# Performance work log

Measured on AMD Instinct MI355X. Metric: run time of the kernel, lower is better.

The kernel has to match this reference:

```python
import jax, jax.numpy as jnp
import numpy as np

B, S, D, H = 2, 2048, 1024, 16
HD = D // H  # head_dim = 64


def setup_inputs() -> dict:
    key = jax.random.key(0)
    ks = jax.random.split(key, 10)
    scale = 0.02
    return {
        "features": jax.random.normal(ks[0], (B, S, D), dtype=jnp.float32),
        "attention_mask": jnp.zeros((B, 1, S, S), dtype=jnp.float32),
        "wq": jax.random.normal(ks[1], (D, D), dtype=jnp.float32) * scale,
        "bq": jnp.zeros((D,), dtype=jnp.float32),
        "wk": jax.random.normal(ks[2], (D, D), dtype=jnp.float32) * scale,
        "bk": jnp.zeros((D,), dtype=jnp.float32),
        "wv": jax.random.normal(ks[3], (D, D), dtype=jnp.float32) * scale,
        "bv": jnp.zeros((D,), dtype=jnp.float32),
        "wo": jax.random.normal(ks[4], (D, D), dtype=jnp.float32) * scale,
        "bo": jnp.zeros((D,), dtype=jnp.float32),
    }


def _split_heads(x):
    # [B,S,D] -> [B,H,S,HD]
    return x.reshape(B, S, H, HD).transpose(0, 2, 1, 3)


def reference(features, attention_mask, wq, bq, wk, bk, wv, bv, wo, bo):
    scaling = HD ** -0.5
    # torch Linear: y = x @ W.T + b; Bart scales q by head_dim**-0.5
    q = _split_heads((features @ wq.T + bq) * scaling)
    k = _split_heads(features @ wk.T + bk)
    v = _split_heads(features @ wv.T + bv)
    scores = jnp.einsum("bhqd,bhkd->bhqk", q, k) + attention_mask
    attn = jax.nn.softmax(scores, axis=-1)
    ctx = jnp.einsum("bhqk,bhkd->bhqd", attn, v)
    ctx = ctx.transpose(0, 2, 1, 3).reshape(B, S, D)
    gated = ctx @ wo.T + bo
    out = features * gated
    return (out, gated)
```

## Files before the change

### kernel.cpp

```cpp
#include <hip/hip_runtime.h>
#include <math.h>

#define Bc 2
#define Sc 2048
#define Dc 1024
#define Hc 16
#define HDc 64
#define NROWS 4096

typedef __attribute__((ext_vector_type(8))) _Float16 f16x8;
typedef __attribute__((ext_vector_type(4))) _Float16 f16x4;
typedef __attribute__((ext_vector_type(2))) __fp16 fp16v2;
typedef __attribute__((ext_vector_type(4))) float f32x4;
typedef __attribute__((ext_vector_type(16))) float f32x16;

__global__ __launch_bounds__(256)
void cvt5(const float* __restrict__ f,  const float* __restrict__ wq,
          const float* __restrict__ wk, const float* __restrict__ wv,
          const float* __restrict__ wo_,
          _Float16* __restrict__ fh, _Float16* __restrict__ wh3,
          _Float16* __restrict__ woh)
{
  int blk = blockIdx.x;
  const float* src; _Float16* hi; int base;
  if (blk < 4096)      { src = f;   hi = fh;            base = blk; }
  else if (blk < 5120) { src = wq;  hi = wh3;           base = blk - 4096; }
  else if (blk < 6144) { src = wk;  hi = wh3 + 1048576; base = blk - 5120; }
  else if (blk < 7168) { src = wv;  hi = wh3 + 2097152; base = blk - 6144; }
  else                 { src = wo_; hi = woh;           base = blk - 7168; }
  int i = base * 256 + threadIdx.x;
  float4 v = reinterpret_cast<const float4*>(src)[i];
  f16x4 h;
  h[0] = (_Float16)v.x; h[1] = (_Float16)v.y;
  h[2] = (_Float16)v.z; h[3] = (_Float16)v.w;
  reinterpret_cast<f16x4*>(hi)[i] = h;
}

__global__ __launch_bounds__(256)
void mask_scan(const float* __restrict__ m, unsigned int* __restrict__ flag)
{
  int i = blockIdx.x * 256 + threadIdx.x;
  float4 v = reinterpret_cast<const float4*>(m)[i];
  bool nz = (v.x != 0.f) || (v.y != 0.f) || (v.z != 0.f) || (v.w != 0.f);
  if (__any(nz)) {
    if ((threadIdx.x & 63) == 0) atomicOr(flag, 1u);
  }
}

__global__ __launch_bounds__(256, 4)
void gemm_qkv(const _Float16* __restrict__ Ah, const _Float16* __restrict__ Wh,
              const float* __restrict__ bq, const float* __restrict__ bk,
              const float* __restrict__ bv,
              _Float16* __restrict__ qb, _Float16* __restrict__ kb,
              _Float16* __restrict__ vtb)
{
  __shared__ _Float16 Ash[128][40];
  __shared__ _Float16 Wsh[128][40];

  const int tid  = threadIdx.x;
  const int lane = tid & 63, wid = tid >> 6;
  const int l15  = lane & 15, l4 = lane >> 4;
  const int wr   = wid >> 1, wc = wid & 1;
  const int arow0 = blockIdx.x * 128;
  const int wrow0 = blockIdx.y * 128;

  f32x4 acc[4][4];
#pragma unroll
  for (int m = 0; m < 4; ++m)
#pragma unroll
    for (int n = 0; n < 4; ++n) acc[m][n] = f32x4{0.f, 0.f, 0.f, 0.f};

  for (int k0 = 0; k0 < Dc; k0 += 32) {
    __syncthreads();
#pragma unroll
    for (int p = 0; p < 2; ++p) {
      int e = tid + 256 * p;
      int r = e >> 2, c8 = (e & 3) * 8;
      *reinterpret_cast<uint4*>(&Ash[r][c8]) =
          *reinterpret_cast<const uint4*>(Ah + (size_t)(arow0 + r) * Dc + k0 + c8);
      *reinterpret_cast<uint4*>(&Wsh[r][c8]) =
          *reinterpret_cast<const uint4*>(Wh + (size_t)(wrow0 + r) * Dc + k0 + c8);
    }
    __syncthreads();

    f16x8 bh[4];
#pragma unroll
    for (int n = 0; n < 4; ++n)
      bh[n] = *reinterpret_cast<const f16x8*>(&Wsh[wc * 64 + n * 16 + l15][l4 * 8]);
#pragma unroll
    for (int m = 0; m < 4; ++m) {
      f16x8 ah = *reinterpret_cast<const f16x8*>(&Ash[wr * 64 + m * 16 + l15][l4 * 8]);
#pragma unroll
      for (int n = 0; n < 4; ++n)
        acc[m][n] = __builtin_amdgcn_mfma_f32_16x16x32_f16(ah, bh[n], acc[m][n], 0, 0, 0);
    }
  }

#pragma unroll
  for (int m = 0; m < 4; ++m) {
#pragma unroll
    for (int n = 0; n < 4; ++n) {
      int cbase = wrow0 + wc * 64 + n * 16;
      int seg = cbase >> 10;
      int o = (cbase & 1023) + l15;
      int h = o >> 6, hd = o & 63;
      const float* bias = (seg == 0) ? bq : ((seg == 1) ? bk : bv);
      float bval = bias[o];
      float alpha = (seg == 0) ? 0.125f : 1.0f;
      int r0 = arow0 + wr * 64 + m * 16 + l4 * 4;
      int b = r0 >> 11, s0 = r0 & (Sc - 1);
      if (seg == 2) {
        f16x4 pk;
#pragma unroll
        for (int reg = 0; reg < 4; ++reg)
          pk[reg] = (_Float16)((acc[m][n][reg] + bval) * alpha);
        *reinterpret_cast<f16x4*>(
            &vtb[(((size_t)b * Hc + h) * HDc + hd) * Sc + s0]) = pk;
      } else {
        _Float16* dst = (seg == 0) ? qb : kb;
#pragma unroll
        for (int reg = 0; reg < 4; ++reg) {
          float val = (acc[m][n][reg] + bval) * alpha;
          dst[(((size_t)b * Hc + h) * Sc + (s0 + reg)) * HDc + hd] = (_Float16)val;
        }
      }
    }
  }
}

__global__ __launch_bounds__(256, 4)
void gemm_wo(const _Float16* __restrict__ Ah, const _Float16* __restrict__ Wh,
             const float* __restrict__ bias,
             float* __restrict__ out0, float* __restrict__ out1,
             const float* __restrict__ feats)
{
  __shared__ _Float16 Ash[64][40];
  __shared__ _Float16 Wsh[128][40];

  const int tid  = threadIdx.x;
  const int lane = tid & 63, wid = tid >> 6;
  const int l15  = lane & 15, l4 = lane >> 4;
  const int wr   = wid >> 1, wc = wid & 1;
  const int arow0 = blockIdx.x * 64;
  const int wrow0 = blockIdx.y * 128;

  f32x4 acc[2][4];
#pragma unroll
  for (int m = 0; m < 2; ++m)
#pragma unroll
    for (int n = 0; n < 4; ++n) acc[m][n] = f32x4{0.f, 0.f, 0.f, 0.f};

  for (int k0 = 0; k0 < Dc; k0 += 32) {
    __syncthreads();
    {
      int r = tid >> 2, c8 = (tid & 3) * 8;
      *reinterpret_cast<uint4*>(&Ash[r][c8]) =
          *reinterpret_cast<const uint4*>(Ah + (size_t)(arow0 + r) * Dc + k0 + c8);
    }
#pragma unroll
    for (int p = 0; p < 2; ++p) {
      int e = tid + 256 * p;
      int r = e >> 2, c8 = (e & 3) * 8;
      *reinterpret_cast<uint4*>(&Wsh[r][c8]) =
          *reinterpret_cast<const uint4*>(Wh + (size_t)(wrow0 + r) * Dc + k0 + c8);
    }
    __syncthreads();

    f16x8 bh[4];
#pragma unroll
    for (int n = 0; n < 4; ++n)
      bh[n] = *reinterpret_cast<const f16x8*>(&Wsh[wc * 64 + n * 16 + l15][l4 * 8]);
#pragma unroll
    for (int m = 0; m < 2; ++m) {
      f16x8 ah = *reinterpret_cast<const f16x8*>(&Ash[wr * 32 + m * 16 + l15][l4 * 8]);
#pragma unroll
      for (int n = 0; n < 4; ++n)
        acc[m][n] = __builtin_amdgcn_mfma_f32_16x16x32_f16(ah, bh[n], acc[m][n], 0, 0, 0);
    }
  }

#pragma unroll
  for (int m = 0; m < 2; ++m) {
#pragma unroll
    for (int n = 0; n < 4; ++n) {
      int c = wrow0 + wc * 64 + n * 16 + l15;
      float bval = bias[c];
#pragma unroll
      for (int reg = 0; reg < 4; ++reg) {
        int r = arow0 + wr * 32 + m * 16 + l4 * 4 + reg;
        float val = acc[m][n][reg] + bval;
        out1[(size_t)r * Dc + c] = val;
        out0[(size_t)r * Dc + c] = feats[(size_t)r * Dc + c] * val;
      }
    }
  }
}

#define QB 128
#define KB 64
#define NT (Sc / KB)

__global__ __launch_bounds__(256, 2)
void attn_mfma(const _Float16* __restrict__ q,
               const _Float16* __restrict__ k,
               const _Float16* __restrict__ vt,
               const float* __restrict__ mask,
               const unsigned int* __restrict__ mflag,
               _Float16* __restrict__ ctxh)
{
  __shared__ _Float16 Ks[2][KB * 64];
  __shared__ _Float16 Vs[2][HDc * 64];

  const int tid  = threadIdx.x;
  const int lane = tid & 63;
  const int wq   = tid >> 6;
  const int l31  = lane & 31;
  const int hi   = lane >> 5;

  const int nqb  = Sc / QB;
  const int bid  = blockIdx.x;
  const int swz  = (bid & 7) * 64 + (bid >> 3);
  const int head = swz / nqb;
  const int q0   = (swz % nqb) * QB;
  const int b    = head / Hc;
  const int h    = head % Hc;

  const bool use_mask = (*mflag != 0u);

  const _Float16* kbase  = k  + (size_t)head * Sc * HDc;
  const _Float16* vtbase = vt + (size_t)head * HDc * Sc;
  const _Float16* qbase  = q  + ((size_t)head * Sc + q0 + wq * 32 + l31) * HDc;
  const float*    ml     = mask + ((size_t)b * Sc + q0 + wq * 32 + l31) * Sc + 4 * hi;

  const int r0s = tid >> 3, cs = tid & 7;
  const int r1s = r0s + 32;
  const int so0 = r0s * 64 + ((cs ^ (r0s & 7)) * 8);
  const int so1 = r1s * 64 + ((cs ^ (r1s & 7)) * 8);

  f16x8 qf[4];
#pragma unroll
  for (int c = 0; c < 4; ++c)
    qf[c] = *reinterpret_cast<const f16x8*>(qbase + hi * 8 + 16 * c);

  f16x8 ones;
#pragma unroll
  for (int i = 0; i < 8; ++i) ones[i] = (_Float16)1.0f;

  f32x16 O0, O1, lacc;
#pragma unroll
  for (int i = 0; i < 16; ++i) { O0[i] = 0.f; O1[i] = 0.f; lacc[i] = 0.f; }
  float m_q = -3e38f;

  *reinterpret_cast<uint4*>(&Ks[0][so0]) =
      *reinterpret_cast<const uint4*>(kbase + (size_t)r0s * HDc + cs * 8);
  *reinterpret_cast<uint4*>(&Ks[0][so1]) =
      *reinterpret_cast<const uint4*>(kbase + (size_t)r1s * HDc + cs * 8);
  *reinterpret_cast<uint4*>(&Vs[0][so0]) =
      *reinterpret_cast<const uint4*>(vtbase + (size_t)r0s * Sc + cs * 8);
  *reinterpret_cast<uint4*>(&Vs[0][so1]) =
      *reinterpret_cast<const uint4*>(vtbase + (size_t)r1s * Sc + cs * 8);
  float4 mpf[8];
  if (use_mask) {
#pragma unroll
    for (int t2 = 0; t2 < 2; ++t2)
#pragma unroll
      for (int j = 0; j < 4; ++j)
        mpf[t2 * 4 + j] = *reinterpret_cast<const float4*>(ml + 32 * t2 + 8 * j);
  }

  for (int kt = 0; kt < NT; ++kt) {
    const int k0 = kt * KB;
    const int cur = kt & 1, nxt = cur ^ 1;
    __syncthreads();

    uint4 kr0, kr1, vr0, vr1;
    const bool pf = (kt + 1) < NT;
    if (pf) {
      const int k1 = k0 + KB;
      kr0 = *reinterpret_cast<const uint4*>(kbase + (size_t)(k1 + r0s) * HDc + cs * 8);
      kr1 = *reinterpret_cast<const uint4*>(kbase + (size_t)(k1 + r1s) * HDc + cs * 8);
      vr0 = *reinterpret_cast<const uint4*>(vtbase + (size_t)r0s * Sc + k1 + cs * 8);
      vr1 = *reinterpret_cast<const uint4*>(vtbase + (size_t)r1s * Sc + k1 + cs * 8);
    }

    f32x16 s[2];
    __builtin_amdgcn_s_setprio(1);
#pragma unroll
    for (int t2 = 0; t2 < 2; ++t2) {
      f32x16 acc;
#pragma unroll
      for (int i = 0; i < 16; ++i) acc[i] = 0.f;
      const int krow = t2 * 32 + l31;
#pragma unroll
      for (int c = 0; c < 4; ++c) {
        const int ofs = krow * 64 + (((2 * c + hi) ^ (krow & 7)) * 8);
        acc = __builtin_amdgcn_mfma_f32_32x32x16_f16(
            *reinterpret_cast<const f16x8*>(&Ks[cur][ofs]), qf[c], acc, 0, 0, 0);
      }
      s[t2] = acc;
    }
    __builtin_amdgcn_s_setprio(0);

    if (use_mask) {
#pragma unroll
      for (int t2 = 0; t2 < 2; ++t2)
#pragma unroll
        for (int j = 0; j < 4; ++j) {
          float4 mv = mpf[t2 * 4 + j];
          s[t2][4 * j + 0] += mv.x; s[t2][4 * j + 1] += mv.y;
          s[t2][4 * j + 2] += mv.z; s[t2][4 * j + 3] += mv.w;
        }
      if (pf) {
#pragma unroll
        for (int t2 = 0; t2 < 2; ++t2)
#pragma unroll
          for (int j = 0; j < 4; ++j)
            mpf[t2 * 4 + j] = *reinterpret_cast<const float4*>(
                ml + (k0 + KB) + 32 * t2 + 8 * j);
      }
    }

    float lm = s[0][0];
#pragma unroll
    for (int t2 = 0; t2 < 2; ++t2)
#pragma unroll
      for (int i = 0; i < 16; ++i) lm = fmaxf(lm, s[t2][i]);

    if (!__all(lm - m_q <= 8.0f)) {
      float vm = fmaxf(lm, __shfl_xor(lm, 32));
      float mn = fmaxf(m_q, vm);
      float cc = __expf(m_q - mn);
      m_q = mn;
#pragma unroll
      for (int reg = 0; reg < 16; ++reg) {
        int q_r = (reg & 3) + 8 * (reg >> 2) + 4 * hi;
        float ccr = __shfl(cc, q_r);
        O0[reg] *= ccr; O1[reg] *= ccr; lacc[reg] *= ccr;
      }
    }

    __builtin_amdgcn_s_setprio(1);
#pragma unroll
    for (int c = 0; c < 4; ++c) {
      const int t2 = c >> 1, rb = (c & 1) * 8;
      float p0 = __expf(s[t2][rb + 0] - m_q);
      float p1 = __expf(s[t2][rb + 1] - m_q);
      float p2 = __expf(s[t2][rb + 2] - m_q);
      float p3 = __expf(s[t2][rb + 3] - m_q);
      float p4 = __expf(s[t2][rb + 4] - m_q);
      float p5 = __expf(s[t2][rb + 5] - m_q);
      float p6 = __expf(s[t2][rb + 6] - m_q);
      float p7 = __expf(s[t2][rb + 7] - m_q);
      union { fp16v2 h; unsigned int u; } w0, w1, w2, w3;
      w0.h = __builtin_amdgcn_cvt_pkrtz(p0, p1);
      w1.h = __builtin_amdgcn_cvt_pkrtz(p2, p3);
      w2.h = __builtin_amdgcn_cvt_pkrtz(p4, p5);
      w3.h = __builtin_amdgcn_cvt_pkrtz(p6, p7);
      unsigned int u0 = w0.u, u1 = w1.u, u2 = w2.u, u3 = w3.u;
      asm("v_permlane32_swap_b32 %0, %1" : "+v"(u0), "+v"(u2));
      asm("v_permlane32_swap_b32 %0, %1" : "+v"(u1), "+v"(u3));
      union { unsigned int u[4]; f16x8 f; } pa;
      pa.u[0] = u0; pa.u[1] = u1; pa.u[2] = u2; pa.u[3] = u3;

      lacc = __builtin_amdgcn_mfma_f32_32x32x16_f16(pa.f, ones, lacc, 0, 0, 0);
      const int vofs = l31 * 64 + (((2 * c + hi) ^ (l31 & 7)) * 8);
      O0 = __builtin_amdgcn_mfma_f32_32x32x16_f16(
          pa.f, *reinterpret_cast<const f16x8*>(&Vs[cur][vofs]), O0, 0, 0, 0);
      O1 = __builtin_amdgcn_mfma_f32_32x32x16_f16(
          pa.f, *reinterpret_cast<const f16x8*>(&Vs[cur][vofs + 32 * 64]), O1, 0, 0, 0);
    }
    __builtin_amdgcn_s_setprio(0);

    if (pf) {
      *reinterpret_cast<uint4*>(&Ks[nxt][so0]) = kr0;
      *reinterpret_cast<uint4*>(&Ks[nxt][so1]) = kr1;
      *reinterpret_cast<uint4*>(&Vs[nxt][so0]) = vr0;
      *reinterpret_cast<uint4*>(&Vs[nxt][so1]) = vr1;
    }
  }

#pragma unroll
  for (int reg = 0; reg < 16; ++reg) {
    int q_r = (reg & 3) + 8 * (reg >> 2) + 4 * hi;
    float inv = 1.0f / lacc[reg];
    size_t rowbase = ((size_t)b * Sc + (q0 + wq * 32 + q_r)) * Dc + h * HDc;
    ctxh[rowbase + l31]      = (_Float16)(O0[reg] * inv);
    ctxh[rowbase + 32 + l31] = (_Float16)(O1[reg] * inv);
  }
}

extern "C" void kernel_launch(void* const* d_in, const int* in_sizes, int n_in,
                              void* d_out, int out_size, void* d_ws, size_t ws_size,
                              hipStream_t stream) {
  const float* feats = (const float*)d_in[0];
  const float* mask  = (const float*)d_in[1];
  const float* wq    = (const float*)d_in[2];
  const float* bq    = (const float*)d_in[3];
  const float* wk    = (const float*)d_in[4];
  const float* bk    = (const float*)d_in[5];
  const float* wv    = (const float*)d_in[6];
  const float* bv    = (const float*)d_in[7];
  const float* wo    = (const float*)d_in[8];
  const float* bo    = (const float*)d_in[9];

  char* ws = (char*)d_ws;
  const size_t MB = (size_t)1 << 20;
  _Float16* fh    = (_Float16*)(ws);
  _Float16* wh3   = (_Float16*)(ws + 8  * MB);
  _Float16* woh   = (_Float16*)(ws + 14 * MB);
  _Float16* qb    = (_Float16*)(ws + 16 * MB);
  _Float16* kb    = (_Float16*)(ws + 24 * MB);
  _Float16* vtb   = (_Float16*)(ws + 32 * MB);
  _Float16* ctxh  = (_Float16*)(ws + 40 * MB);
  unsigned int* mflag = (unsigned int*)(ws + 48 * MB);

  float* out   = (float*)d_out;
  float* gated = out + 4194304;

  hipMemsetAsync(mflag, 0, 4, stream);
  mask_scan<<<8192, 256, 0, stream>>>(mask, mflag);

  cvt5<<<8192, 256, 0, stream>>>(feats, wq, wk, wv, wo, fh, wh3, woh);

  gemm_qkv<<<dim3(NROWS / 128, 3072 / 128), 256, 0, stream>>>(
      fh, wh3, bq, bk, bv, qb, kb, vtb);

  attn_mfma<<<Bc * Hc * (Sc / QB), 256, 0, stream>>>(qb, kb, vtb, mask, mflag, ctxh);

  gemm_wo<<<dim3(NROWS / 64, Dc / 128), 256, 0, stream>>>(
      ctxh, woh, bo, out, gated, feats);
}
```

Baseline: 150.1 us.

## Fuse mask scan into conversion kernel and halve attention query block

The mask-nonzero scan is merged into the fp16 conversion kernel, so one launch does both jobs and a kernel boundary goes away. The attention kernel moves from 128-query blocks with 4 waves to 64-query blocks with 2 waves, doubling the grid to 1024 blocks. The block swizzle and the K/V tile load loop change to match, with each thread now loading 4 rows instead of 2. The aim is better CU occupancy and load balance for attention, at the cost of reloading K/V tiles more often per query.

```diff
diff --git a/kernel.cpp b/kernel.cpp
--- a/kernel.cpp
+++ b/kernel.cpp
@@ -15,11 +15,11 @@
 typedef __attribute__((ext_vector_type(16))) float f32x16;
 
 __global__ __launch_bounds__(256)
-void cvt5(const float* __restrict__ f,  const float* __restrict__ wq,
+void prep(const float* __restrict__ f,  const float* __restrict__ wq,
           const float* __restrict__ wk, const float* __restrict__ wv,
-          const float* __restrict__ wo_,
+          const float* __restrict__ wo_, const float* __restrict__ mask,
           _Float16* __restrict__ fh, _Float16* __restrict__ wh3,
-          _Float16* __restrict__ woh)
+          _Float16* __restrict__ woh, unsigned int* __restrict__ flag)
 {
   int blk = blockIdx.x;
   const float* src; _Float16* hi; int base;
@@ -34,14 +34,10 @@
   h[0] = (_Float16)v.x; h[1] = (_Float16)v.y;
   h[2] = (_Float16)v.z; h[3] = (_Float16)v.w;
   reinterpret_cast<f16x4*>(hi)[i] = h;
-}
-
-__global__ __launch_bounds__(256)
-void mask_scan(const float* __restrict__ m, unsigned int* __restrict__ flag)
-{
-  int i = blockIdx.x * 256 + threadIdx.x;
-  float4 v = reinterpret_cast<const float4*>(m)[i];
-  bool nz = (v.x != 0.f) || (v.y != 0.f) || (v.z != 0.f) || (v.w != 0.f);
+
+  int g = blk * 256 + threadIdx.x;
+  float4 mv = reinterpret_cast<const float4*>(mask)[g];
+  bool nz = (mv.x != 0.f) || (mv.y != 0.f) || (mv.z != 0.f) || (mv.w != 0.f);
   if (__any(nz)) {
     if ((threadIdx.x & 63) == 0) atomicOr(flag, 1u);
   }
@@ -196,11 +192,11 @@
   }
 }
 
-#define QB 128
+#define QB 64
 #define KB 64
 #define NT (Sc / KB)
 
-__global__ __launch_bounds__(256, 2)
+__global__ __launch_bounds__(128, 2)
 void attn_mfma(const _Float16* __restrict__ q,
                const _Float16* __restrict__ k,
                const _Float16* __restrict__ vt,
@@ -219,7 +215,7 @@
 
   const int nqb  = Sc / QB;
   const int bid  = blockIdx.x;
-  const int swz  = (bid & 7) * 64 + (bid >> 3);
+  const int swz  = (bid & 7) * 128 + (bid >> 3);
   const int head = swz / nqb;
   const int q0   = (swz % nqb) * QB;
   const int b    = head / Hc;
@@ -232,10 +228,13 @@
   const _Float16* qbase  = q  + ((size_t)head * Sc + q0 + wq * 32 + l31) * HDc;
   const float*    ml     = mask + ((size_t)b * Sc + q0 + wq * 32 + l31) * Sc + 4 * hi;
 
-  const int r0s = tid >> 3, cs = tid & 7;
-  const int r1s = r0s + 32;
-  const int so0 = r0s * 64 + ((cs ^ (r0s & 7)) * 8);
-  const int so1 = r1s * 64 + ((cs ^ (r1s & 7)) * 8);
+  const int rs = tid >> 3, cs = tid & 7;
+  int so[4];
+#pragma unroll
+  for (int p = 0; p < 4; ++p) {
+    int r = rs + 16 * p;
+    so[p] = r * 64 + ((cs ^ (r & 7)) * 8);
+  }
 
   f16x8 qf[4];
 #pragma unroll
@@ -251,14 +250,14 @@
   for (int i = 0; i < 16; ++i) { O0[i] = 0.f; O1[i] = 0.f; lacc[i] = 0.f; }
   float m_q = -3e38f;
 
-  *reinterpret_cast<uint4*>(&Ks[0][so0]) =
-      *reinterpret_cast<const uint4*>(kbase + (size_t)r0s * HDc + cs * 8);
-  *reinterpret_cast<uint4*>(&Ks[0][so1]) =
-      *reinterpret_cast<const uint4*>(kbase + (size_t)r1s * HDc + cs * 8);
-  *reinterpret_cast<uint4*>(&Vs[0][so0]) =
-      *reinterpret_cast<const uint4*>(vtbase + (size_t)r0s * Sc + cs * 8);
-  *reinterpret_cast<uint4*>(&Vs[0][so1]) =
-      *reinterpret_cast<const uint4*>(vtbase + (size_t)r1s * Sc + cs * 8);
+#pragma unroll
+  for (int p = 0; p < 4; ++p) {
+    int r = rs + 16 * p;
+    *reinterpret_cast<uint4*>(&Ks[0][so[p]]) =
+        *reinterpret_cast<const uint4*>(kbase + (size_t)r * HDc + cs * 8);
+    *reinterpret_cast<uint4*>(&Vs[0][so[p]]) =
+        *reinterpret_cast<const uint4*>(vtbase + (size_t)r * Sc + cs * 8);
+  }
   float4 mpf[8];
   if (use_mask) {
 #pragma unroll
@@ -273,14 +272,16 @@
     const int cur = kt & 1, nxt = cur ^ 1;
     __syncthreads();
 
-    uint4 kr0, kr1, vr0, vr1;
+    uint4 kr[4], vr[4];
     const bool pf = (kt + 1) < NT;
     if (pf) {
       const int k1 = k0 + KB;
-      kr0 = *reinterpret_cast<const uint4*>(kbase + (size_t)(k1 + r0s) * HDc + cs * 8);
-      kr1 = *reinterpret_cast<const uint4*>(kbase + (size_t)(k1 + r1s) * HDc + cs * 8);
-      vr0 = *reinterpret_cast<const uint4*>(vtbase + (size_t)r0s * Sc + k1 + cs * 8);
-      vr1 = *reinterpret_cast<const uint4*>(vtbase + (size_t)r1s * Sc + k1 + cs * 8);
+#pragma unroll
+      for (int p = 0; p < 4; ++p) {
+        int r = rs + 16 * p;
+        kr[p] = *reinterpret_cast<const uint4*>(kbase + (size_t)(k1 + r) * HDc + cs * 8);
+        vr[p] = *reinterpret_cast<const uint4*>(vtbase + (size_t)r * Sc + k1 + cs * 8);
+      }
     }
 
     f32x16 s[2];
@@ -372,10 +373,11 @@
     __builtin_amdgcn_s_setprio(0);
 
     if (pf) {
-      *reinterpret_cast<uint4*>(&Ks[nxt][so0]) = kr0;
-      *reinterpret_cast<uint4*>(&Ks[nxt][so1]) = kr1;
-      *reinterpret_cast<uint4*>(&Vs[nxt][so0]) = vr0;
-      *reinterpret_cast<uint4*>(&Vs[nxt][so1]) = vr1;
+#pragma unroll
+      for (int p = 0; p < 4; ++p) {
+        *reinterpret_cast<uint4*>(&Ks[nxt][so[p]]) = kr[p];
+        *reinterpret_cast<uint4*>(&Vs[nxt][so[p]]) = vr[p];
+      }
     }
   }
 
@@ -418,14 +420,14 @@
   float* gated = out + 4194304;
 
   hipMemsetAsync(mflag, 0, 4, stream);
-  mask_scan<<<8192, 256, 0, stream>>>(mask, mflag);
-
-  cvt5<<<8192, 256, 0, stream>>>(feats, wq, wk, wv, wo, fh, wh3, woh);
+
+  prep<<<8192, 256, 0, stream>>>(feats, wq, wk, wv, wo, mask,
+                                 fh, wh3, woh, mflag);
 
   gemm_qkv<<<dim3(NROWS / 128, 3072 / 128), 256, 0, stream>>>(
       fh, wh3, bq, bk, bv, qb, kb, vtb);
 
-  attn_mfma<<<Bc * Hc * (Sc / QB), 256, 0, stream>>>(qb, kb, vtb, mask, mflag, ctxh);
+  attn_mfma<<<Bc * Hc * (Sc / QB), 128, 0, stream>>>(qb, kb, vtb, mask, mflag, ctxh);
 
   gemm_wo<<<dim3(NROWS / 64, Dc / 128), 256, 0, stream>>>(
       ctxh, woh, bo, out, gated, feats);
```

New measurement: 157.2 us. +4.8%, slower.
